# Kernel tuning notes

Hardware: AMD Instinct MI355X
Metric: run time of the kernel (lower is better)

Reference implementation:

```python
import jax, jax.numpy as jnp
import numpy as np

# High-pass biquad coefficients from the original module
A_HP = (-1.99599, 0.996)
B_HP = (-2.0, 1.0)


def _biquad(x, b0, b1, a0, a1):
    """Direct-form-II-transposed biquad over time axis.
    x: [B, T]; coefficients are scalars; zero initial state (fresh buffers).
    """
    B = x.shape[0]
    init = (jnp.zeros((B,), x.dtype), jnp.zeros((B,), x.dtype))

    def step(mem, xi):  # xi: [B]
        m0, m1 = mem
        yi = xi + m0
        new_m0 = m1 + b0 * xi - a0 * yi
        new_m1 = b1 * xi - a1 * yi
        return (new_m0, new_m1), yi

    _, y = jax.lax.scan(step, init, x.T)  # scan over T
    return y.T  # [B, T]


def setup_inputs() -> dict:
    key = jax.random.key(0)
    kx, kn, k1, k2, k3, k4 = jax.random.split(key, 6)
    B, T = 4096, 16000
    x = jax.random.normal(kx, (B, T), dtype=jnp.float32)
    n = jax.random.normal(kn, (B, T), dtype=jnp.float32)
    # _rand_resp: 0.75 * (uniform[0,1) - 0.5), shape [batch]
    rr = lambda k: (0.75 * (jax.random.uniform(k, (B,), dtype=jnp.float32) - 0.5))
    return {"x": x, "n": n, "a_x": rr(k1), "b_x": rr(k2), "a_n": rr(k3), "b_n": rr(k4)}


def reference(x, n, a_x, b_x, a_n, b_n):
    # Signal path: fixed high-pass biquad, then random-response biquad.
    # NOTE (faithful to source): b[0], b[1] / a[0], a[1] index the BATCH-sized
    # random vectors, i.e. only the first two entries act as coefficients.
    x = _biquad(x, B_HP[0], B_HP[1], A_HP[0], A_HP[1])
    x = _biquad(x, b_x[0], b_x[1], a_x[0], a_x[1])
    n = _biquad(n, B_HP[0], B_HP[1], A_HP[0], A_HP[1])
    n = _biquad(n, b_n[0], b_n[1], a_n[0], a_n[1])
    return (x, n)
```

## Files before the change

kernel.cpp:

```cpp
#include <hip/hip_runtime.h>

#define T_LEN 16000
#define HALF  8000
#define SEG_L 33
#define NSEG  243
#define ROWS  4096

#define HP_NA0  1.99599f
#define HP_NA1 -0.996f
#define HP_B0  -2.0f
#define HP_B1   1.0f

__device__ __forceinline__ void mm4(const float* A, const float* B, float* C) {
#pragma unroll
  for (int r = 0; r < 4; ++r) {
#pragma unroll
    for (int c = 0; c < 4; ++c) {
      float s = 0.f;
#pragma unroll
      for (int k = 0; k < 4; ++k) s = fmaf(A[r * 4 + k], B[k * 4 + c], s);
      C[r * 4 + c] = s;
    }
  }
}

__global__ void setup_kernel(const float* __restrict__ a_x, const float* __restrict__ b_x,
                             const float* __restrict__ a_n, const float* __restrict__ b_n,
                             float* __restrict__ ws) {
  int p = threadIdx.x;
  if (p >= 2) return;
  const float* a = p ? a_n : a_x;
  const float* b = p ? b_n : b_x;
  float a0 = a[0], a1 = a[1], b0 = b[0], b1 = b[1];

  float M[16] = {
      HP_NA0,   1.f, 0.f,  0.f,
      HP_NA1,   0.f, 0.f,  0.f,
      b0 - a0,  0.f, -a0,  1.f,
      b1 - a1,  0.f, -a1,  0.f};

  float res[16], tmp[16];
#pragma unroll
  for (int i = 0; i < 16; ++i) res[i] = M[i];
  for (int s = 1; s < SEG_L; ++s) {
    mm4(res, M, tmp);
#pragma unroll
    for (int i = 0; i < 16; ++i) res[i] = tmp[i];
  }
  float* dst = ws + p * 128;
#pragma unroll
  for (int i = 0; i < 16; ++i) dst[i] = res[i];
  for (int k = 1; k < 8; ++k) {
    mm4(res, res, tmp);
#pragma unroll
    for (int i = 0; i < 16; ++i) { res[i] = tmp[i]; dst[k * 16 + i] = res[i]; }
  }
}

__launch_bounds__(256)
__global__ void filt_kernel(const float* __restrict__ x, const float* __restrict__ n,
                            const float* __restrict__ a_x, const float* __restrict__ b_x,
                            const float* __restrict__ a_n, const float* __restrict__ b_n,
                            const float* __restrict__ ws, float* __restrict__ out) {
  __shared__ float  buf[HALF];
  __shared__ float4 sd[2][NSEG];
  __shared__ float  Pm[128];
  __shared__ float  carry[4];

  const int bid = blockIdx.x;
  const int path = bid >> 12;
  const int row = bid & 4095;
  const int t = threadIdx.x;

  const float* src = (path ? n : x) + (size_t)row * T_LEN;
  float* dst = out + (size_t)path * ((size_t)ROWS * T_LEN) + (size_t)row * T_LEN;

  if (t < 128) Pm[t] = ws[path * 128 + t];

  const float* aa = path ? a_n : a_x;
  const float* bb = path ? b_n : b_x;
  const float a0r = aa[0], a1r = aa[1], b0r = bb[0], b1r = bb[1];
  const float na0r = -a0r, na1r = -a1r;

  float i0 = 0.f, i1 = 0.f, i2 = 0.f, i3 = 0.f;

  for (int h = 0; h < 2; ++h) {
    const float* hsrc = src + h * HALF;

    {
      const float4* s4 = reinterpret_cast<const float4*>(hsrc);
      float4* b4 = reinterpret_cast<float4*>(buf);
      for (int i = t; i < HALF / 4; i += 256) b4[i] = s4[i];
    }
    __syncthreads();

    float p0 = 0.f, p1 = 0.f, q0 = 0.f, q1 = 0.f;
    if (t < NSEG) {
      if (t == 0) { p0 = i0; p1 = i1; q0 = i2; q1 = i3; }
      const int base = t * SEG_L;
      for (int j = 0; j < SEG_L; ++j) {
        const int idx = base + j;
        const float xv = (idx < HALF) ? buf[idx] : 0.f;
        const float y1 = xv + p0;
        const float np0 = fmaf(HP_NA0, y1, fmaf(HP_B0, xv, p1));
        p1 = fmaf(HP_NA1, y1, HP_B1 * xv);
        p0 = np0;
        const float y2 = y1 + q0;
        const float nq0 = fmaf(na0r, y2, fmaf(b0r, y1, q1));
        q1 = fmaf(na1r, y2, b1r * y1);
        q0 = nq0;
      }
      sd[0][t] = make_float4(p0, p1, q0, q1);
    }
    __syncthreads();

    float4 d = make_float4(p0, p1, q0, q1);
    int cur = 0;
    for (int k = 0; k < 8; ++k) {
      const int o = 1 << k;
      if (t < NSEG) {
        if (t >= o) {
          const float4 v = sd[cur][t - o];
          const float* P = Pm + k * 16;
          d.x = fmaf(P[0],  v.x, fmaf(P[1],  v.y, fmaf(P[2],  v.z, fmaf(P[3],  v.w, d.x))));
          d.y = fmaf(P[4],  v.x, fmaf(P[5],  v.y, fmaf(P[6],  v.z, fmaf(P[7],  v.w, d.y))));
          d.z = fmaf(P[8],  v.x, fmaf(P[9],  v.y, fmaf(P[10], v.z, fmaf(P[11], v.w, d.z))));
          d.w = fmaf(P[12], v.x, fmaf(P[13], v.y, fmaf(P[14], v.z, fmaf(P[15], v.w, d.w))));
        }
        sd[cur ^ 1][t] = d;
      }
      cur ^= 1;
      __syncthreads();
    }

    if (t < NSEG) {
      float sp0 = i0, sp1 = i1, sq0 = i2, sq1 = i3;
      if (t > 0) {
        const float4 v = sd[0][t - 1];
        sp0 = v.x; sp1 = v.y; sq0 = v.z; sq1 = v.w;
      }
      const int base = t * SEG_L;
      const int lim = min(SEG_L, HALF - base);
      for (int j = 0; j < lim; ++j) {
        const int idx = base + j;
        const float xv = buf[idx];
        const float y1 = xv + sp0;
        const float np0 = fmaf(HP_NA0, y1, fmaf(HP_B0, xv, sp1));
        sp1 = fmaf(HP_NA1, y1, HP_B1 * xv);
        sp0 = np0;
        const float y2 = y1 + sq0;
        const float nq0 = fmaf(na0r, y2, fmaf(b0r, y1, sq1));
        sq1 = fmaf(na1r, y2, b1r * y1);
        sq0 = nq0;
        buf[idx] = y2;
      }
      if (t == NSEG - 1) {
        carry[0] = sp0; carry[1] = sp1; carry[2] = sq0; carry[3] = sq1;
      }
    }
    __syncthreads();

    {
      float4* d4 = reinterpret_cast<float4*>(dst) + h * (HALF / 4);
      const float4* b4 = reinterpret_cast<const float4*>(buf);
      for (int i = t; i < HALF / 4; i += 256) d4[i] = b4[i];
    }
    i0 = carry[0]; i1 = carry[1]; i2 = carry[2]; i3 = carry[3];
    __syncthreads();
  }
}

extern "C" void kernel_launch(void* const* d_in, const int* in_sizes, int n_in,
                              void* d_out, int out_size, void* d_ws, size_t ws_size,
                              hipStream_t stream) {
  const float* x   = (const float*)d_in[0];
  const float* n   = (const float*)d_in[1];
  const float* a_x = (const float*)d_in[2];
  const float* b_x = (const float*)d_in[3];
  const float* a_n = (const float*)d_in[4];
  const float* b_n = (const float*)d_in[5];
  float* out = (float*)d_out;
  float* ws  = (float*)d_ws;

  hipLaunchKernelGGL(setup_kernel, dim3(1), dim3(64), 0, stream, a_x, b_x, a_n, b_n, ws);
  hipLaunchKernelGGL(filt_kernel, dim3(2 * ROWS), dim3(256), 0, stream,
                     x, n, a_x, b_x, a_n, b_n, ws, out);
}
```

Before: 851.2 us.

## Process rows in quarter chunks to cut LDS and raise occupancy

Each block now streams its row in four 4000-sample chunks instead of two 8000-sample halves. This roughly halves the shared-memory buffer and reduces segments to 122 and scan steps to 7. Launch bounds now request 8 blocks per CU, aiming for more resident blocks to hide memory latency. The cost is more chunk iterations, more barriers per row, and only about half of the 256 threads doing scan work; the final read of sd also moves to the correct ping-pong buffer for an odd step count.

```diff
diff --git a/kernel.cpp b/kernel.cpp
--- a/kernel.cpp
+++ b/kernel.cpp
@@ -1,10 +1,11 @@
 #include <hip/hip_runtime.h>
 
-#define T_LEN 16000
-#define HALF  8000
-#define SEG_L 33
-#define NSEG  243
-#define ROWS  4096
+#define T_LEN   16000
+#define QUART   4000
+#define SEG_L   33
+#define NSEG    122
+#define NSTEPS  7
+#define ROWS    4096
 
 #define HP_NA0  1.99599f
 #define HP_NA1 -0.996f
@@ -50,21 +51,21 @@
   float* dst = ws + p * 128;
 #pragma unroll
   for (int i = 0; i < 16; ++i) dst[i] = res[i];
-  for (int k = 1; k < 8; ++k) {
+  for (int k = 1; k < NSTEPS; ++k) {
     mm4(res, res, tmp);
 #pragma unroll
     for (int i = 0; i < 16; ++i) { res[i] = tmp[i]; dst[k * 16 + i] = res[i]; }
   }
 }
 
-__launch_bounds__(256)
+__launch_bounds__(256, 8)
 __global__ void filt_kernel(const float* __restrict__ x, const float* __restrict__ n,
                             const float* __restrict__ a_x, const float* __restrict__ b_x,
                             const float* __restrict__ a_n, const float* __restrict__ b_n,
                             const float* __restrict__ ws, float* __restrict__ out) {
-  __shared__ float  buf[HALF];
+  __shared__ float  buf[QUART];
   __shared__ float4 sd[2][NSEG];
-  __shared__ float  Pm[128];
+  __shared__ float  Pm[NSTEPS * 16];
   __shared__ float  carry[4];
 
   const int bid = blockIdx.x;
@@ -75,7 +76,7 @@
   const float* src = (path ? n : x) + (size_t)row * T_LEN;
   float* dst = out + (size_t)path * ((size_t)ROWS * T_LEN) + (size_t)row * T_LEN;
 
-  if (t < 128) Pm[t] = ws[path * 128 + t];
+  if (t < NSTEPS * 16) Pm[t] = ws[path * 128 + t];
 
   const float* aa = path ? a_n : a_x;
   const float* bb = path ? b_n : b_x;
@@ -84,13 +85,11 @@
 
   float i0 = 0.f, i1 = 0.f, i2 = 0.f, i3 = 0.f;
 
-  for (int h = 0; h < 2; ++h) {
-    const float* hsrc = src + h * HALF;
-
+  for (int h = 0; h < 4; ++h) {
     {
-      const float4* s4 = reinterpret_cast<const float4*>(hsrc);
+      const float4* s4 = reinterpret_cast<const float4*>(src) + h * (QUART / 4);
       float4* b4 = reinterpret_cast<float4*>(buf);
-      for (int i = t; i < HALF / 4; i += 256) b4[i] = s4[i];
+      for (int i = t; i < QUART / 4; i += 256) b4[i] = s4[i];
     }
     __syncthreads();
 
@@ -100,7 +99,7 @@
       const int base = t * SEG_L;
       for (int j = 0; j < SEG_L; ++j) {
         const int idx = base + j;
-        const float xv = (idx < HALF) ? buf[idx] : 0.f;
+        const float xv = (idx < QUART) ? buf[idx] : 0.f;
         const float y1 = xv + p0;
         const float np0 = fmaf(HP_NA0, y1, fmaf(HP_B0, xv, p1));
         p1 = fmaf(HP_NA1, y1, HP_B1 * xv);
@@ -116,7 +115,7 @@
 
     float4 d = make_float4(p0, p1, q0, q1);
     int cur = 0;
-    for (int k = 0; k < 8; ++k) {
+    for (int k = 0; k < NSTEPS; ++k) {
       const int o = 1 << k;
       if (t < NSEG) {
         if (t >= o) {
@@ -136,11 +135,11 @@
     if (t < NSEG) {
       float sp0 = i0, sp1 = i1, sq0 = i2, sq1 = i3;
       if (t > 0) {
-        const float4 v = sd[0][t - 1];
+        const float4 v = sd[cur][t - 1];
         sp0 = v.x; sp1 = v.y; sq0 = v.z; sq1 = v.w;
       }
       const int base = t * SEG_L;
-      const int lim = min(SEG_L, HALF - base);
+      const int lim = min(SEG_L, QUART - base);
       for (int j = 0; j < lim; ++j) {
         const int idx = base + j;
         const float xv = buf[idx];
@@ -161,9 +160,9 @@
     __syncthreads();
 
     {
-      float4* d4 = reinterpret_cast<float4*>(dst) + h * (HALF / 4);
+      float4* d4 = reinterpret_cast<float4*>(dst) + h * (QUART / 4);
       const float4* b4 = reinterpret_cast<const float4*>(buf);
-      for (int i = t; i < HALF / 4; i += 256) d4[i] = b4[i];
+      for (int i = t; i < QUART / 4; i += 256) d4[i] = b4[i];
     }
     i0 = carry[0]; i1 = carry[1]; i2 = carry[2]; i3 = carry[3];
     __syncthreads();
```

New measurement: 861.2 us. About the same (+1.2%).
